# Optimization experiments

Hardware: AMD Instinct MI355X
Metric: run time of the kernel (lower is better)

Reference implementation:

```python
import jax, jax.numpy as jnp
import numpy as np

P = 0.3            # swap probability (matches init_kwargs p)
H = 224
W = 224
PERM_SEED = 42     # fixed key so the reference is deterministic


def _index_permute(key, h, w, p):
    """Sequential random-neighbor swap permutation over an h*w grid.

    Faithful to CLOPLayer._index_permute: visit all flat indices in a random
    order; for each, with prob p swap it with one of its 4 toroidal neighbors
    (each with prob p/4). Implemented as a lax.scan over the visitation order
    (the swaps are inherently sequential / order-dependent).
    """
    n = h * w
    k1, k2 = jax.random.split(key)
    order = jax.random.permutation(k1, n)                       # visitation order
    probs = jnp.array([1.0 - p, p / 4, p / 4, p / 4, p / 4], dtype=jnp.float32)
    rs = jax.random.choice(k2, 5, shape=(n,), p=probs)          # move type per step

    def step(indexes, inp):
        idx, r = inp
        i = idx // w
        j = idx % w
        ip = jnp.where(r == 1, (i + 1) % h, jnp.where(r == 2, (i - 1) % h, i))
        jp = jnp.where(r == 3, (j + 1) % w, jnp.where(r == 4, (j - 1) % w, j))
        idx2 = jnp.where(r == 0, idx, ip * w + jp)              # r==0 -> self-swap (no-op)
        a = indexes[idx]
        b = indexes[idx2]
        indexes = indexes.at[idx].set(b).at[idx2].set(a)
        return indexes, None

    indexes = jnp.arange(n, dtype=jnp.int32)
    indexes, _ = jax.lax.scan(step, indexes, (order.astype(jnp.int32), rs.astype(jnp.int32)))
    return indexes


def setup_inputs() -> dict:
    key = jax.random.key(0)
    x = jax.random.normal(key, (128, 3, H, W), dtype=jnp.float32)
    return {"x": x}


def reference(x) -> jnp.ndarray:
    b, c, h, w = x.shape
    idx = _index_permute(jax.random.key(PERM_SEED), h, w, P)     # [h*w] int32
    flat = x.reshape(b, c, h * w)
    # torch.gather(flat, 2, idx broadcast over b,c) == take along last axis
    res = jnp.take(flat, idx, axis=2)
    return res.reshape(b, c, h, w)
```

## Files before the change

kernel.cpp:

```cpp
#include <hip/hip_runtime.h>
#include <cstdint>
#include <cstring>
#include <vector>
#include <algorithm>


#define PH 224
#define PW 224
#define PN (PH * PW)
#define NBC (128 * 3)
#define BC_PER_BLOCK 8

static inline uint32_t rotl32(uint32_t v, int d) {
  return (v << d) | (v >> (32 - d));
}

static void tf2x32(uint32_t k0, uint32_t k1, uint32_t x0, uint32_t x1,
                   uint32_t& o0, uint32_t& o1) {
  const uint32_t ks0 = k0, ks1 = k1, ks2 = k0 ^ k1 ^ 0x1BD11BDAu;
  uint32_t v0 = x0 + ks0;
  uint32_t v1 = x1 + ks1;
  static const int ra[4] = {13, 15, 26, 6};
  static const int rb[4] = {17, 29, 16, 24};
#define R4(rr)                              \
  do {                                      \
    for (int _i = 0; _i < 4; ++_i) {        \
      v0 += v1;                             \
      v1 = rotl32(v1, (rr)[_i]);            \
      v1 ^= v0;                             \
    }                                       \
  } while (0)
  R4(ra); v0 += ks1; v1 += ks2 + 1u;
  R4(rb); v0 += ks2; v1 += ks0 + 2u;
  R4(ra); v0 += ks0; v1 += ks1 + 3u;
  R4(rb); v0 += ks1; v1 += ks2 + 4u;
  R4(ra); v0 += ks2; v1 += ks0 + 5u;
#undef R4
  o0 = v0;
  o1 = v1;
}

static void jax_split2(uint32_t k0, uint32_t k1,
                       uint32_t& a0, uint32_t& a1, uint32_t& b0, uint32_t& b1) {
  tf2x32(k0, k1, 0u, 0u, a0, a1);
  tf2x32(k0, k1, 0u, 1u, b0, b1);
}

static inline uint32_t jax_rb32(uint32_t k0, uint32_t k1, uint32_t i) {
  uint32_t y0, y1;
  tf2x32(k0, k1, 0u, i, y0, y1);
  return y0 ^ y1;
}

static std::vector<int> compute_perm() {
  const int n = PN;
  const uint32_t K0 = 0u, K1 = 42u;

  uint32_t k1a, k1b, k2a, k2b;
  jax_split2(K0, K1, k1a, k1b, k2a, k2b);

  std::vector<int> order(n);
  for (int i = 0; i < n; ++i) order[i] = i;
  uint32_t ck0 = k1a, ck1 = k1b;
  std::vector<std::pair<uint32_t, int>> kv(n);
  for (int round = 0; round < 2; ++round) {
    uint32_t nk0, nk1, sk0, sk1;
    jax_split2(ck0, ck1, nk0, nk1, sk0, sk1);
    ck0 = nk0; ck1 = nk1;
    for (int i = 0; i < n; ++i) {
      kv[i] = {jax_rb32(sk0, sk1, (uint32_t)i), order[i]};
    }
    std::stable_sort(kv.begin(), kv.end(),
                     [](const std::pair<uint32_t, int>& a,
                        const std::pair<uint32_t, int>& b) {
                       return a.first < b.first;
                     });
    for (int i = 0; i < n; ++i) order[i] = kv[i].second;
  }

  float probs[5] = {(float)(1.0 - 0.3), (float)(0.3 / 4), (float)(0.3 / 4),
                    (float)(0.3 / 4), (float)(0.3 / 4)};
  float pc[5];
  pc[0] = probs[0];
  for (int i = 1; i < 5; ++i) pc[i] = pc[i - 1] + probs[i];

  std::vector<uint8_t> rs(n);
  for (int i = 0; i < n; ++i) {
    uint32_t bits = jax_rb32(k2a, k2b, (uint32_t)i);
    uint32_t fb = (bits >> 9) | 0x3f800000u;
    float u;
    std::memcpy(&u, &fb, 4);
    u -= 1.0f;
    if (u < 0.0f) u = 0.0f;
    float r = pc[4] * (1.0f - u);
    int ind = (int)(std::lower_bound(pc, pc + 5, r) - pc);
    rs[i] = (uint8_t)ind;
  }

  std::vector<int> idx(n);
  for (int i = 0; i < n; ++i) idx[i] = i;
  for (int t = 0; t < n; ++t) {
    const int id = order[t];
    const int r = rs[t];
    const int i = id / PW, j = id % PW;
    int ip = i, jp = j;
    if (r == 1)      ip = (i + 1) % PH;
    else if (r == 2) ip = (i - 1 + PH) % PH;
    else if (r == 3) jp = (j + 1) % PW;
    else if (r == 4) jp = (j - 1 + PW) % PW;
    const int id2 = (r == 0) ? id : (ip * PW + jp);
    const int a = idx[id];
    const int b = idx[id2];
    idx[id]  = b;
    idx[id2] = a;
  }
  return idx;
}

struct PermHolder {
  std::vector<int> h_idx;
  int* d_idx = nullptr;
  PermHolder() {
    h_idx = compute_perm();
    int* p = nullptr;
    if (hipMalloc(&p, PN * sizeof(int)) == hipSuccess) {
      if (hipMemcpy(p, h_idx.data(), PN * sizeof(int),
                    hipMemcpyHostToDevice) == hipSuccess) {
        d_idx = p;
      }
    }
  }
};
static PermHolder g_perm;

__global__ __launch_bounds__(256) void clop_gather(
    const float* __restrict__ x, const int* __restrict__ idx,
    float* __restrict__ out) {
  const int k = blockIdx.x * 256 + threadIdx.x;
  const int s = idx[k];
  const int bc0 = blockIdx.y * BC_PER_BLOCK;
#pragma unroll
  for (int t = 0; t < BC_PER_BLOCK; ++t) {
    const size_t bc = (size_t)(bc0 + t);
    out[bc * PN + k] = x[bc * PN + s];
  }
}

extern "C" void kernel_launch(void* const* d_in, const int* in_sizes, int n_in,
                              void* d_out, int out_size, void* d_ws,
                              size_t ws_size, hipStream_t stream) {
  const float* x = (const float*)d_in[0];
  float* out = (float*)d_out;

  const int* idx;
  if (g_perm.d_idx != nullptr) {
    idx = g_perm.d_idx;
  } else {
    hipMemcpyAsync(d_ws, g_perm.h_idx.data(), PN * sizeof(int),
                   hipMemcpyHostToDevice, stream);
    idx = (const int*)d_ws;
  }

  dim3 grid(PN / 256, NBC / BC_PER_BLOCK);
  clop_gather<<<grid, 256, 0, stream>>>(x, idx, out);
}
```

Measured before the change: 140.3 us.

## Stage row windows with halo in LDS and gather from shared memory

Adds a kernel that loads a 56-row output window plus an 8-row toroidal halo of each image plane into LDS using vectorized loads. It then performs the permutation gather from LDS with precomputed 16-bit local offsets and writes vectorized nontemporal stores. The goal is to replace scattered global reads with coalesced loads, at the cost of re-reading halo rows and about 64KB of LDS per block. If any source falls outside the halo the host check fails and the code falls back to the old gather kernel.

```diff
diff --git a/kernel.cpp b/kernel.cpp
--- a/kernel.cpp
+++ b/kernel.cpp
@@ -9,7 +9,15 @@
 #define PW 224
 #define PN (PH * PW)
 #define NBC (128 * 3)
-#define BC_PER_BLOCK 8
+
+#define R_OUT 56
+#define HALO 8
+#define S_ROWS (R_OUT + 2 * HALO)
+#define NWIN (PH / R_OUT)
+#define KWIN (R_OUT * PW)
+
+typedef float f4v __attribute__((ext_vector_type(4)));
+typedef unsigned short u4v __attribute__((ext_vector_type(4)));
 
 static inline uint32_t rotl32(uint32_t v, int d) {
   return (v << d) | (v >> (32 - d));
@@ -22,7 +30,7 @@
   uint32_t v1 = x1 + ks1;
   static const int ra[4] = {13, 15, 26, 6};
   static const int rb[4] = {17, 29, 16, 24};
-#define R4(rr)                              \
+#define R4X(rr)                             \
   do {                                      \
     for (int _i = 0; _i < 4; ++_i) {        \
       v0 += v1;                             \
@@ -30,12 +38,12 @@
       v1 ^= v0;                             \
     }                                       \
   } while (0)
-  R4(ra); v0 += ks1; v1 += ks2 + 1u;
-  R4(rb); v0 += ks2; v1 += ks0 + 2u;
-  R4(ra); v0 += ks0; v1 += ks1 + 3u;
-  R4(rb); v0 += ks1; v1 += ks2 + 4u;
-  R4(ra); v0 += ks2; v1 += ks0 + 5u;
-#undef R4
+  R4X(ra); v0 += ks1; v1 += ks2 + 1u;
+  R4X(rb); v0 += ks2; v1 += ks0 + 2u;
+  R4X(ra); v0 += ks0; v1 += ks1 + 3u;
+  R4X(rb); v0 += ks1; v1 += ks2 + 4u;
+  R4X(ra); v0 += ks2; v1 += ks0 + 5u;
+#undef R4X
   o0 = v0;
   o1 = v1;
 }
@@ -119,29 +127,90 @@
 
 struct PermHolder {
   std::vector<int> h_idx;
+  std::vector<uint16_t> h_lofs;
   int* d_idx = nullptr;
+  uint16_t* d_lofs = nullptr;
+  bool lds_ok = false;
+
   PermHolder() {
     h_idx = compute_perm();
+
+    h_lofs.assign((size_t)NWIN * KWIN, 0);
+    bool ok = true;
+    for (int w = 0; w < NWIN && ok; ++w) {
+      const int g0 = w * R_OUT - HALO;
+      for (int kk = 0; kk < KWIN; ++kk) {
+        const int k = w * KWIN + kk;
+        const int s = h_idx[k];
+        const int srow = s / PW, scol = s % PW;
+        int i = ((srow - g0) % PH + PH) % PH;
+        if (i >= S_ROWS) { ok = false; break; }
+        h_lofs[(size_t)w * KWIN + kk] = (uint16_t)(i * PW + scol);
+      }
+    }
+
     int* p = nullptr;
-    if (hipMalloc(&p, PN * sizeof(int)) == hipSuccess) {
-      if (hipMemcpy(p, h_idx.data(), PN * sizeof(int),
+    if (hipMalloc(&p, PN * sizeof(int)) == hipSuccess &&
+        hipMemcpy(p, h_idx.data(), PN * sizeof(int),
+                  hipMemcpyHostToDevice) == hipSuccess) {
+      d_idx = p;
+    }
+    if (ok) {
+      uint16_t* q = nullptr;
+      if (hipMalloc(&q, (size_t)NWIN * KWIN * sizeof(uint16_t)) == hipSuccess &&
+          hipMemcpy(q, h_lofs.data(), (size_t)NWIN * KWIN * sizeof(uint16_t),
                     hipMemcpyHostToDevice) == hipSuccess) {
-        d_idx = p;
+        d_lofs = q;
+        lds_ok = true;
       }
     }
   }
 };
 static PermHolder g_perm;
+
+__global__ __launch_bounds__(256) void clop_lds(
+    const float* __restrict__ x, const uint16_t* __restrict__ lofs,
+    float* __restrict__ out) {
+  __shared__ float tile[S_ROWS * PW];
+
+  const int w = blockIdx.x;
+  const size_t bc = blockIdx.y;
+  const int g0 = w * R_OUT - HALO;
+  const float* xs = x + bc * PN;
+
+  for (int t = threadIdx.x; t < S_ROWS * (PW / 4); t += 256) {
+    const int i = t / (PW / 4);
+    const int j = (t % (PW / 4)) * 4;
+    int g = g0 + i;
+    if (g < 0) g += PH;
+    else if (g >= PH) g -= PH;
+    const f4v v = *(const f4v*)(xs + g * PW + j);
+    *(f4v*)(tile + i * PW + j) = v;
+  }
+  __syncthreads();
+
+  const uint16_t* lw = lofs + (size_t)w * KWIN;
+  float* ob = out + bc * PN + (size_t)w * KWIN;
+  for (int t = threadIdx.x; t < KWIN / 4; t += 256) {
+    const u4v o4 = *(const u4v*)(lw + t * 4);
+    f4v v;
+    v.x = tile[o4.x];
+    v.y = tile[o4.y];
+    v.z = tile[o4.z];
+    v.w = tile[o4.w];
+    __builtin_nontemporal_store(v, (f4v*)(ob + t * 4));
+  }
+}
 
 __global__ __launch_bounds__(256) void clop_gather(
     const float* __restrict__ x, const int* __restrict__ idx,
     float* __restrict__ out) {
   const int k = blockIdx.x * 256 + threadIdx.x;
   const int s = idx[k];
-  const int bc0 = blockIdx.y * BC_PER_BLOCK;
+  const size_t bc0 = (size_t)blockIdx.y * 8;
 #pragma unroll
-  for (int t = 0; t < BC_PER_BLOCK; ++t) {
-    const size_t bc = (size_t)(bc0 + t);
+  for (int t = 0; t < 8; ++t) {
+    const size_t bc = bc0 + t;
     out[bc * PN + k] = x[bc * PN + s];
   }
 }
@@ -152,15 +221,20 @@
   const float* x = (const float*)d_in[0];
   float* out = (float*)d_out;
 
+  if (g_perm.lds_ok) {
+    dim3 grid(NWIN, NBC);
+    clop_lds<<<grid, 256, 0, stream>>>(x, g_perm.d_lofs, out);
+    return;
+  }
+
   const int* idx;
   if (g_perm.d_idx != nullptr) {
     idx = g_perm.d_idx;
   } else {
-    hipMemcpyAsync(d_ws, g_perm.h_idx.data(), PN * sizeof(int),
-                   hipMemcpyHostToDevice, stream);
+    (void)hipMemcpyAsync(d_ws, g_perm.h_idx.data(), PN * sizeof(int),
+                         hipMemcpyHostToDevice, stream);
     idx = (const int*)d_ws;
   }
-
-  dim3 grid(PN / 256, NBC / BC_PER_BLOCK);
+  dim3 grid(PN / 256, NBC / 8);
   clop_gather<<<grid, 256, 0, stream>>>(x, idx, out);
 }
```

Result: slower. 153.4 us (+9.3%).
